# Optimization experiments

Measured on AMD Instinct MI355X. Metric: run time of the kernel, lower is better.

The kernel has to match this reference:

```python
import jax, jax.numpy as jnp
import numpy as np

N, E = 50000, 1600000
IN, OUT, H = 128, 32, 2
NT, ET = 20, 4
ETE, EAE, ED = 16, 16, 16
SLOPE = 0.2  # conv_neg_slope


def setup_inputs() -> dict:
    key = jax.random.key(0)
    ks = jax.random.split(key, 11)
    d_att = 2 * OUT + ETE + EAE
    return dict(
        x=jax.random.normal(ks[0], (N, IN), jnp.float32),
        edge_index=jax.random.randint(ks[1], (2, E), 0, N),
        ntypes=jax.random.randint(ks[2], (N,), 0, NT),
        etypes=jax.random.randint(ks[3], (E,), 0, ET),
        eattr=jax.random.normal(ks[4], (E, ED), jnp.float32),
        het_W=jax.random.normal(ks[5], (NT, IN, OUT), jnp.float32) / np.sqrt(IN).astype(np.float32),
        het_b=jnp.zeros((NT, OUT), jnp.float32),
        etype_table=jax.random.normal(ks[6], (ET, ETE), jnp.float32),
        eattr_W=jax.random.normal(ks[7], (ED, EAE), jnp.float32) / np.sqrt(ED).astype(np.float32),
        att_W=jax.random.normal(ks[8], (d_att, H), jnp.float32) / np.sqrt(d_att).astype(np.float32),
        lin_W=jax.random.normal(ks[9], (OUT + EAE, OUT), jnp.float32) / np.sqrt(OUT + EAE).astype(np.float32),
    )


def _lrelu(v):
    return jax.nn.leaky_relu(v, SLOPE)


def _heat_conv(x, edge_index, ntypes, etypes, eattr,
               het_W, het_b, etype_table, eattr_W, att_W, lin_W):
    # HeteroLinear: node-type-conditioned linear transform (loop over 20 types,
    # avoids materializing a [N, IN, OUT] gathered-weight tensor)
    h = jnp.zeros((x.shape[0], het_W.shape[-1]), x.dtype)
    for t in range(het_W.shape[0]):
        h = h + jnp.where((ntypes == t)[:, None], x @ het_W[t] + het_b[t], 0.0)

    src, dst = edge_index[0], edge_index[1]
    ete = _lrelu(etype_table[etypes])        # [E, ETE] edge-type embedding
    ea = _lrelu(eattr @ eattr_W)             # [E, EAE] edge-attr embedding
    x_i = h[dst]                             # target node feats [E, OUT]
    x_j = h[src]                             # source node feats [E, OUT]

    feat = jnp.concatenate([x_i, x_j, ete, ea], axis=-1)
    alpha = _lrelu(feat @ att_W)             # [E, H] raw attention logits

    # softmax grouped by destination node, per head
    amax = jax.ops.segment_max(alpha, dst, num_segments=N)  # [N, H]
    alpha = jnp.exp(alpha - amax[dst])
    denom = jax.ops.segment_sum(alpha, dst, num_segments=N)  # [N, H]
    alpha = alpha / denom[dst]

    msg = jnp.concatenate([x_j, ea], axis=-1) @ lin_W        # [E, OUT]
    m = (msg[:, None, :] * alpha[:, :, None]).reshape(alpha.shape[0], H * OUT)
    out = jax.ops.segment_sum(m, dst, num_segments=N)        # [N, H*OUT]
    return out  # concat=True -> flattened heads


def reference(x, edge_index, ntypes, etypes, eattr,
              het_W, het_b, etype_table, eattr_W, att_W, lin_W):
    out = _heat_conv(x, edge_index, ntypes, etypes, eattr,
                     het_W, het_b, etype_table, eattr_W, att_W, lin_W)
    return jax.nn.relu(out)  # final activation in forward (eval mode: no dropout)
```

## Files before the change

kernel.cpp:

```cpp
#include <hip/hip_runtime.h>
#include <hip/hip_fp16.h>

#define NN 50000
#define EE 1600000
#define IN_F 128
#define SLOPE 0.2f
#define NB_SCAN 196
#define NPAD 16

__global__ __launch_bounds__(256) void k_node(
    const float* __restrict__ x, const int* __restrict__ ntypes,
    const float* __restrict__ hetW, const float* __restrict__ hetb,
    const float* __restrict__ linW, const float* __restrict__ attW,
    float* __restrict__ hlin, float* __restrict__ auxS,
    float* __restrict__ auxD)
{
    __shared__ float sH[32 * 33];
    __shared__ float sLin[32 * 32];
    int tid = threadIdx.x;
    for (int i = tid; i < 1024; i += 256) sLin[i] = linW[i];

    int g = tid >> 3;
    int j = tid & 7;
    int n = blockIdx.x * 32 + g;
    int nc = n < NN ? n : NN - 1;
    int t = ntypes[nc];
    const float* W = hetW + (size_t)t * (IN_F * 32);
    const float4* xr = (const float4*)(x + (size_t)nc * IN_F);

    float4 acc = ((const float4*)(hetb + t * 32))[j];
    #pragma unroll 4
    for (int c = 0; c < 32; ++c) {
        float4 xv = xr[c];
        const float* Wr = W + (4 * c) * 32 + 4 * j;
        float4 w0 = *(const float4*)(Wr);
        float4 w1 = *(const float4*)(Wr + 32);
        float4 w2 = *(const float4*)(Wr + 64);
        float4 w3 = *(const float4*)(Wr + 96);
        acc.x += xv.x * w0.x + xv.y * w1.x + xv.z * w2.x + xv.w * w3.x;
        acc.y += xv.x * w0.y + xv.y * w1.y + xv.z * w2.y + xv.w * w3.y;
        acc.z += xv.x * w0.z + xv.y * w1.z + xv.z * w2.z + xv.w * w3.z;
        acc.w += xv.x * w0.w + xv.y * w1.w + xv.z * w2.w + xv.w * w3.w;
    }
    sH[g * 33 + 4 * j + 0] = acc.x;
    sH[g * 33 + 4 * j + 1] = acc.y;
    sH[g * 33 + 4 * j + 2] = acc.z;
    sH[g * 33 + 4 * j + 3] = acc.w;
    __syncthreads();

    int o = tid & 31;
    #pragma unroll
    for (int pass = 0; pass < 4; ++pass) {
        int g2 = (tid >> 5) + 8 * pass;
        int n2 = blockIdx.x * 32 + g2;
        if (n2 >= NN) break;
        float accl = 0.0f;
        #pragma unroll
        for (int k = 0; k < 32; ++k)
            accl += sH[g2 * 33 + k] * sLin[k * 32 + o];
        hlin[(size_t)n2 * 32 + o] = accl;

        float hv = sH[g2 * 33 + o];
        float p0 = hv * attW[o * 2],        p1 = hv * attW[o * 2 + 1];
        float p2 = hv * attW[(32 + o) * 2], p3 = hv * attW[(32 + o) * 2 + 1];
        #pragma unroll
        for (int m = 16; m >= 1; m >>= 1) {
            p0 += __shfl_xor(p0, m, 32);
            p1 += __shfl_xor(p1, m, 32);
            p2 += __shfl_xor(p2, m, 32);
            p3 += __shfl_xor(p3, m, 32);
        }
        if (o == 0) {
            auxD[n2 * 2] = p0; auxD[n2 * 2 + 1] = p1;
            auxS[n2 * 2] = p2; auxS[n2 * 2 + 1] = p3;
        }
    }
}

__global__ __launch_bounds__(256) void k_count(
    const int* __restrict__ dst, int* __restrict__ count)
{
    int e = blockIdx.x * 256 + threadIdx.x;
    atomicAdd(&count[dst[e]], 1);
}

__global__ __launch_bounds__(256) void k_scanA(
    const int* __restrict__ count, int* __restrict__ offsets,
    int* __restrict__ bsum)
{
    __shared__ int s[256];
    int t = threadIdx.x;
    int i = blockIdx.x * 256 + t;
    int c = (i < NN) ? count[i] : 0;
    s[t] = c;
    __syncthreads();
    for (int off = 1; off < 256; off <<= 1) {
        int v = (t >= off) ? s[t - off] : 0;
        __syncthreads();
        s[t] += v;
        __syncthreads();
    }
    if (i < NN) offsets[i] = s[t] - c;
    if (t == 255) bsum[blockIdx.x] = s[255];
}

__global__ __launch_bounds__(256) void k_scanB(
    const int* __restrict__ bsum, int* __restrict__ bbase,
    const float* __restrict__ etab, const float* __restrict__ attW,
    float* __restrict__ etedot)
{
    __shared__ int s[256];
    int t = threadIdx.x;
    if (t < 8) {
        int et = t >> 1, hh = t & 1;
        float acc = 0.0f;
        for (int k = 0; k < 16; ++k) {
            float v = etab[et * 16 + k];
            v = v > 0.0f ? v : SLOPE * v;
            acc += v * attW[(64 + k) * 2 + hh];
        }
        etedot[t] = acc;
    }
    int c = (t < NB_SCAN) ? bsum[t] : 0;
    s[t] = c;
    __syncthreads();
    for (int off = 1; off < 256; off <<= 1) {
        int v = (t >= off) ? s[t - off] : 0;
        __syncthreads();
        s[t] += v;
        __syncthreads();
    }
    if (t < NB_SCAN) bbase[t] = s[t] - c;
}

__global__ __launch_bounds__(256) void k_scanC(
    int* __restrict__ offsets, const int* __restrict__ bbase,
    int* __restrict__ nextPad)
{
    int t = threadIdx.x;
    int i = blockIdx.x * 256 + t;
    if (i < NN) {
        int v = offsets[i] + bbase[blockIdx.x];
        offsets[i] = v;
        nextPad[i * NPAD] = v;
    }
    if (i == 0) offsets[NN] = EE;
}

__global__ __launch_bounds__(256) void k_pre3(
    const int* __restrict__ srcp, const int* __restrict__ dstp,
    const int* __restrict__ etypes, const float* __restrict__ eattr,
    const float* __restrict__ eaW, const float* __restrict__ attW,
    const float* __restrict__ linW, const float* __restrict__ etedot,
    const float* __restrict__ auxS, const float* __restrict__ auxD,
    int* __restrict__ nextPad, __half* __restrict__ eaLinBuf,
    int2* __restrict__ recB)
{
    int e = blockIdx.x * 256 + threadIdx.x;
    int s = srcp[e], d = dstp[e], et = etypes[e];
    int slot = atomicAdd(&nextPad[d * NPAD], 1);

    float attr[16];
    {
        const float4* ap = (const float4*)(eattr + (size_t)e * 16);
        #pragma unroll
        for (int q = 0; q < 4; ++q) {
            float4 v = ap[q];
            attr[4*q+0] = v.x; attr[4*q+1] = v.y;
            attr[4*q+2] = v.z; attr[4*q+3] = v.w;
        }
    }
    float ea[16];
    #pragma unroll
    for (int j = 0; j < 16; ++j) {
        float acc = 0.0f;
        #pragma unroll
        for (int k = 0; k < 16; ++k) acc += attr[k] * eaW[k * 16 + j];
        ea[j] = acc > 0.0f ? acc : SLOPE * acc;
    }

    float2 aD = ((const float2*)auxD)[d];
    float2 aS = ((const float2*)auxS)[s];
    float2 eD = ((const float2*)etedot)[et];
    float al0 = aD.x + aS.x + eD.x;
    float al1 = aD.y + aS.y + eD.y;
    #pragma unroll
    for (int j = 0; j < 16; ++j) {
        al0 += ea[j] * attW[(80 + j) * 2];
        al1 += ea[j] * attW[(80 + j) * 2 + 1];
    }
    al0 = al0 > 0.0f ? al0 : SLOPE * al0;
    al1 = al1 > 0.0f ? al1 : SLOPE * al1;
    float p0 = __expf(al0), p1 = __expf(al1);

    float ml[32];
    #pragma unroll
    for (int o = 0; o < 32; ++o) ml[o] = 0.0f;
    #pragma unroll
    for (int j = 0; j < 16; ++j) {
        float ej = ea[j];
        #pragma unroll
        for (int o = 0; o < 32; ++o) ml[o] += ej * linW[(32 + j) * 32 + o];
    }

    __half2 mh[16];
    #pragma unroll
    for (int q = 0; q < 16; ++q)
        mh[q] = __floats2half2_rn(ml[2*q], ml[2*q+1]);
    float4* P = (float4*)(eaLinBuf + (size_t)slot * 32);
    const float4* ms = (const float4*)mh;
    #pragma unroll
    for (int q = 0; q < 4; ++q) P[q] = ms[q];

    __half2 ph = __floats2half2_rn(p0, p1);
    recB[slot] = make_int2(s, *(const int*)&ph);
}

__global__ __launch_bounds__(256) void k_gather3(
    const int* __restrict__ offsets, const __half* __restrict__ eaLinBuf,
    const int2* __restrict__ recB, const float* __restrict__ hlin,
    float* __restrict__ out)
{
    int tid = blockIdx.x * 256 + threadIdx.x;
    int n = tid >> 6;
    int lane = tid & 63;
    if (n >= NN) return;
    int o = lane & 31, hh = lane >> 5;
    int s0 = offsets[n], s1 = offsets[n + 1];

    float accm = 0.0f, accp = 0.0f;
    int slot = s0;
    for (; slot + 3 < s1; slot += 4) {
        int2 r0 = recB[slot + 0];
        int2 r1 = recB[slot + 1];
        int2 r2 = recB[slot + 2];
        int2 r3 = recB[slot + 3];
        float el0 = __half2float(eaLinBuf[(size_t)(slot + 0) * 32 + o]);
        float el1 = __half2float(eaLinBuf[(size_t)(slot + 1) * 32 + o]);
        float el2 = __half2float(eaLinBuf[(size_t)(slot + 2) * 32 + o]);
        float el3 = __half2float(eaLinBuf[(size_t)(slot + 3) * 32 + o]);
        float hv0 = hlin[(size_t)r0.x * 32 + o];
        float hv1 = hlin[(size_t)r1.x * 32 + o];
        float hv2 = hlin[(size_t)r2.x * 32 + o];
        float hv3 = hlin[(size_t)r3.x * 32 + o];
        __half2 q0 = *(const __half2*)&r0.y;
        __half2 q1 = *(const __half2*)&r1.y;
        __half2 q2 = *(const __half2*)&r2.y;
        __half2 q3 = *(const __half2*)&r3.y;
        float p0 = hh ? __high2float(q0) : __low2float(q0);
        float p1 = hh ? __high2float(q1) : __low2float(q1);
        float p2 = hh ? __high2float(q2) : __low2float(q2);
        float p3 = hh ? __high2float(q3) : __low2float(q3);
        accm += p0 * (hv0 + el0);
        accm += p1 * (hv1 + el1);
        accm += p2 * (hv2 + el2);
        accm += p3 * (hv3 + el3);
        accp += (p0 + p1) + (p2 + p3);
    }
    for (; slot < s1; ++slot) {
        int2 r = recB[slot];
        float el = __half2float(eaLinBuf[(size_t)slot * 32 + o]);
        float hv = hlin[(size_t)r.x * 32 + o];
        __half2 q = *(const __half2*)&r.y;
        float p = hh ? __high2float(q) : __low2float(q);
        accm += p * (hv + el);
        accp += p;
    }
    float v = accp > 0.0f ? accm / accp : 0.0f;
    out[(size_t)n * 64 + lane] = v > 0.0f ? v : 0.0f;
}

extern "C" void kernel_launch(void* const* d_in, const int* in_sizes, int n_in,
                              void* d_out, int out_size, void* d_ws, size_t ws_size,
                              hipStream_t stream)
{
    const float* x      = (const float*)d_in[0];
    const int*   eidx   = (const int*)  d_in[1];
    const int*   ntypes = (const int*)  d_in[2];
    const int*   etypes = (const int*)  d_in[3];
    const float* eattr  = (const float*)d_in[4];
    const float* hetW   = (const float*)d_in[5];
    const float* hetb   = (const float*)d_in[6];
    const float* etab   = (const float*)d_in[7];
    const float* eaW    = (const float*)d_in[8];
    const float* attW   = (const float*)d_in[9];
    const float* linW   = (const float*)d_in[10];
    float* out = (float*)d_out;

    char* ws = (char*)d_ws;
    size_t off = 0;
    auto alloc = [&](size_t bytes) {
        char* p = ws + off;
        off = (off + bytes + 255) & ~(size_t)255;
        return p;
    };
    float*  hlin     = (float*) alloc((size_t)NN * 32 * sizeof(float));
    float*  auxS     = (float*) alloc((size_t)NN * 2 * sizeof(float));
    float*  auxD     = (float*) alloc((size_t)NN * 2 * sizeof(float));
    float*  etedot   = (float*) alloc(8 * sizeof(float));
    int*    count    = (int*)   alloc((size_t)NN * sizeof(int));
    int*    offsets  = (int*)   alloc(((size_t)NN + 1) * sizeof(int));
    int*    nextPad  = (int*)   alloc((size_t)NN * NPAD * sizeof(int));
    int*    bsum     = (int*)   alloc(256 * sizeof(int));
    int*    bbase    = (int*)   alloc(256 * sizeof(int));
    int2*   recB     = (int2*)  alloc((size_t)EE * sizeof(int2));
    __half* eaLinBuf = (__half*)alloc((size_t)EE * 32 * sizeof(__half));
    (void)ws_size;

    const int* srcp = eidx;
    const int* dstp = eidx + EE;

    hipMemsetAsync(count, 0, (size_t)NN * sizeof(int), stream);

    k_node<<<(NN + 31) / 32, 256, 0, stream>>>(x, ntypes, hetW, hetb, linW,
                                               attW, hlin, auxS, auxD);
    k_count<<<EE / 256, 256, 0, stream>>>(dstp, count);
    k_scanA<<<NB_SCAN, 256, 0, stream>>>(count, offsets, bsum);
    k_scanB<<<1, 256, 0, stream>>>(bsum, bbase, etab, attW, etedot);
    k_scanC<<<NB_SCAN, 256, 0, stream>>>(offsets, bbase, nextPad);
    k_pre3<<<EE / 256, 256, 0, stream>>>(srcp, dstp, etypes, eattr, eaW, attW,
                                         linW, etedot, auxS, auxD, nextPad,
                                         eaLinBuf, recB);
    k_gather3<<<(NN * 64 + 255) / 256, 256, 0, stream>>>(offsets, eaLinBuf,
                                                         recB, hlin, out);
}
```

Baseline: 491.3 us.

## Store edge embedding instead of projected message; apply linW in gather via fdot2

The pre-pass now stores the 16-dim fp16 edge-attribute embedding plus the source index and attention weights in one 64-byte padded record per edge, instead of a 32-dim fp16 projected message and a separate 8-byte record. The gather kernel recomputes the eattr-to-message projection per lane with packed fp16 dot products, using linW columns held in registers. The aim is to shrink the scatter write and merge two streams into one aligned record, moving the projection arithmetic into the gather. The record is padded to 64 bytes, so the per-edge footprint stays close to before, and the fp16 weights add rounding error.

Result: slower. 577.8 us (+17.6%).

```diff
diff --git a/kernel.cpp b/kernel.cpp
--- a/kernel.cpp
+++ b/kernel.cpp
@@ -7,6 +7,8 @@
 #define SLOPE 0.2f
 #define NB_SCAN 196
 #define NPAD 16
+
+typedef _Float16 hf2 __attribute__((ext_vector_type(2)));
 
 __global__ __launch_bounds__(256) void k_node(
     const float* __restrict__ x, const int* __restrict__ ntypes,
@@ -147,14 +149,13 @@
     if (i == 0) offsets[NN] = EE;
 }
 
-__global__ __launch_bounds__(256) void k_pre3(
+__global__ __launch_bounds__(256) void k_pre4(
     const int* __restrict__ srcp, const int* __restrict__ dstp,
     const int* __restrict__ etypes, const float* __restrict__ eattr,
     const float* __restrict__ eaW, const float* __restrict__ attW,
-    const float* __restrict__ linW, const float* __restrict__ etedot,
-    const float* __restrict__ auxS, const float* __restrict__ auxD,
-    int* __restrict__ nextPad, __half* __restrict__ eaLinBuf,
-    int2* __restrict__ recB)
+    const float* __restrict__ etedot, const float* __restrict__ auxS,
+    const float* __restrict__ auxD, int* __restrict__ nextPad,
+    float4* __restrict__ recBuf)
 {
     int e = blockIdx.x * 256 + threadIdx.x;
     int s = srcp[e], d = dstp[e], et = etypes[e];
@@ -193,32 +194,27 @@
     al1 = al1 > 0.0f ? al1 : SLOPE * al1;
     float p0 = __expf(al0), p1 = __expf(al1);
 
-    float ml[32];
-    #pragma unroll
-    for (int o = 0; o < 32; ++o) ml[o] = 0.0f;
-    #pragma unroll
-    for (int j = 0; j < 16; ++j) {
-        float ej = ea[j];
-        #pragma unroll
-        for (int o = 0; o < 32; ++o) ml[o] += ej * linW[(32 + j) * 32 + o];
-    }
-
-    __half2 mh[16];
-    #pragma unroll
-    for (int q = 0; q < 16; ++q)
-        mh[q] = __floats2half2_rn(ml[2*q], ml[2*q+1]);
-    float4* P = (float4*)(eaLinBuf + (size_t)slot * 32);
-    const float4* ms = (const float4*)mh;
-    #pragma unroll
-    for (int q = 0; q < 4; ++q) P[q] = ms[q];
-
+    __half2 eh[8];
+    #pragma unroll
+    for (int q = 0; q < 8; ++q)
+        eh[q] = __floats2half2_rn(ea[2*q], ea[2*q+1]);
     __half2 ph = __floats2half2_rn(p0, p1);
-    recB[slot] = make_int2(s, *(const int*)&ph);
-}
-
-__global__ __launch_bounds__(256) void k_gather3(
-    const int* __restrict__ offsets, const __half* __restrict__ eaLinBuf,
-    const int2* __restrict__ recB, const float* __restrict__ hlin,
+
+    float4* P = recBuf + (size_t)slot * 4;
+    P[0] = ((const float4*)eh)[0];
+    P[1] = ((const float4*)eh)[1];
+    float4 m;
+    ((int*)&m)[0] = s;
+    ((int*)&m)[1] = *(const int*)&ph;
+    ((int*)&m)[2] = 0;
+    ((int*)&m)[3] = 0;
+    P[2] = m;
+    P[3] = make_float4(0.f, 0.f, 0.f, 0.f);
+}
+
+__global__ __launch_bounds__(256) void k_gather4(
+    const int* __restrict__ offsets, const float4* __restrict__ recBuf,
+    const float* __restrict__ hlin, const float* __restrict__ linW,
     float* __restrict__ out)
 {
     int tid = blockIdx.x * 256 + threadIdx.x;
@@ -226,45 +222,64 @@
     int lane = tid & 63;
     if (n >= NN) return;
     int o = lane & 31, hh = lane >> 5;
+
+    hf2 wcol[8];
+    #pragma unroll
+    for (int q = 0; q < 8; ++q) {
+        float wa = linW[(32 + 2 * q) * 32 + o];
+        float wb = linW[(33 + 2 * q) * 32 + o];
+        hf2 w; w[0] = (_Float16)wa; w[1] = (_Float16)wb;
+        wcol[q] = w;
+    }
+
     int s0 = offsets[n], s1 = offsets[n + 1];
-
     float accm = 0.0f, accp = 0.0f;
     int slot = s0;
-    for (; slot + 3 < s1; slot += 4) {
-        int2 r0 = recB[slot + 0];
-        int2 r1 = recB[slot + 1];
-        int2 r2 = recB[slot + 2];
-        int2 r3 = recB[slot + 3];
-        float el0 = __half2float(eaLinBuf[(size_t)(slot + 0) * 32 + o]);
-        float el1 = __half2float(eaLinBuf[(size_t)(slot + 1) * 32 + o]);
-        float el2 = __half2float(eaLinBuf[(size_t)(slot + 2) * 32 + o]);
-        float el3 = __half2float(eaLinBuf[(size_t)(slot + 3) * 32 + o]);
-        float hv0 = hlin[(size_t)r0.x * 32 + o];
-        float hv1 = hlin[(size_t)r1.x * 32 + o];
-        float hv2 = hlin[(size_t)r2.x * 32 + o];
-        float hv3 = hlin[(size_t)r3.x * 32 + o];
-        __half2 q0 = *(const __half2*)&r0.y;
-        __half2 q1 = *(const __half2*)&r1.y;
-        __half2 q2 = *(const __half2*)&r2.y;
-        __half2 q3 = *(const __half2*)&r3.y;
-        float p0 = hh ? __high2float(q0) : __low2float(q0);
-        float p1 = hh ? __high2float(q1) : __low2float(q1);
-        float p2 = hh ? __high2float(q2) : __low2float(q2);
-        float p3 = hh ? __high2float(q3) : __low2float(q3);
-        accm += p0 * (hv0 + el0);
-        accm += p1 * (hv1 + el1);
-        accm += p2 * (hv2 + el2);
-        accm += p3 * (hv3 + el3);
-        accp += (p0 + p1) + (p2 + p3);
+    for (; slot + 1 < s1; slot += 2) {
+        float4 a0 = recBuf[(size_t)slot * 4 + 0];
+        float4 a1 = recBuf[(size_t)slot * 4 + 1];
+        int2   ma = *(const int2*)(recBuf + (size_t)slot * 4 + 2);
+        float4 b0 = recBuf[(size_t)(slot + 1) * 4 + 0];
+        float4 b1 = recBuf[(size_t)(slot + 1) * 4 + 1];
+        int2   mb = *(const int2*)(recBuf + (size_t)(slot + 1) * 4 + 2);
+        float hva = hlin[(size_t)ma.x * 32 + o];
+        float hvb = hlin[(size_t)mb.x * 32 + o];
+
+        union { float4 f; hf2 h[4]; } ua0, ua1, ub0, ub1;
+        ua0.f = a0; ua1.f = a1; ub0.f = b0; ub1.f = b1;
+        float ea0 = 0.f, ea1 = 0.f, eb0 = 0.f, eb1 = 0.f;
+        #pragma unroll
+        for (int q = 0; q < 4; ++q) {
+            ea0 = __builtin_amdgcn_fdot2(ua0.h[q], wcol[q],     ea0, false);
+            ea1 = __builtin_amdgcn_fdot2(ua1.h[q], wcol[4 + q], ea1, false);
+            eb0 = __builtin_amdgcn_fdot2(ub0.h[q], wcol[q],     eb0, false);
+            eb1 = __builtin_amdgcn_fdot2(ub1.h[q], wcol[4 + q], eb1, false);
+        }
+        __half2 qa = *(const __half2*)&ma.y;
+        __half2 qb = *(const __half2*)&mb.y;
+        float pa = hh ? __high2float(qa) : __low2float(qa);
+        float pb = hh ? __high2float(qb) : __low2float(qb);
+        accm += pa * (hva + ea0 + ea1);
+        accm += pb * (hvb + eb0 + eb1);
+        accp += pa + pb;
     }
     for (; slot < s1; ++slot) {
-        int2 r = recB[slot];
-        float el = __half2float(eaLinBuf[(size_t)slot * 32 + o]);
-        float hv = hlin[(size_t)r.x * 32 + o];
-        __half2 q = *(const __half2*)&r.y;
-        float p = hh ? __high2float(q) : __low2float(q);
-        accm += p * (hv + el);
-        accp += p;
+        float4 a0 = recBuf[(size_t)slot * 4 + 0];
+        float4 a1 = recBuf[(size_t)slot * 4 + 1];
+        int2   ma = *(const int2*)(recBuf + (size_t)slot * 4 + 2);
+        float hva = hlin[(size_t)ma.x * 32 + o];
+        union { float4 f; hf2 h[4]; } ua0, ua1;
+        ua0.f = a0; ua1.f = a1;
+        float e0 = 0.f, e1 = 0.f;
+        #pragma unroll
+        for (int q = 0; q < 4; ++q) {
+            e0 = __builtin_amdgcn_fdot2(ua0.h[q], wcol[q],     e0, false);
+            e1 = __builtin_amdgcn_fdot2(ua1.h[q], wcol[4 + q], e1, false);
+        }
+        __half2 qa = *(const __half2*)&ma.y;
+        float pa = hh ? __high2float(qa) : __low2float(qa);
+        accm += pa * (hva + e0 + e1);
+        accp += pa;
     }
     float v = accp > 0.0f ? accm / accp : 0.0f;
     out[(size_t)n * 64 + lane] = v > 0.0f ? v : 0.0f;
@@ -303,8 +318,7 @@
     int*    nextPad  = (int*)   alloc((size_t)NN * NPAD * sizeof(int));
     int*    bsum     = (int*)   alloc(256 * sizeof(int));
     int*    bbase    = (int*)   alloc(256 * sizeof(int));
-    int2*   recB     = (int2*)  alloc((size_t)EE * sizeof(int2));
-    __half* eaLinBuf = (__half*)alloc((size_t)EE * 32 * sizeof(__half));
+    float4* recBuf   = (float4*)alloc((size_t)EE * 64);
     (void)ws_size;
 
     const int* srcp = eidx;
@@ -318,9 +332,8 @@
     k_scanA<<<NB_SCAN, 256, 0, stream>>>(count, offsets, bsum);
     k_scanB<<<1, 256, 0, stream>>>(bsum, bbase, etab, attW, etedot);
     k_scanC<<<NB_SCAN, 256, 0, stream>>>(offsets, bbase, nextPad);
-    k_pre3<<<EE / 256, 256, 0, stream>>>(srcp, dstp, etypes, eattr, eaW, attW,
-                                         linW, etedot, auxS, auxD, nextPad,
-                                         eaLinBuf, recB);
-    k_gather3<<<(NN * 64 + 255) / 256, 256, 0, stream>>>(offsets, eaLinBuf,
-                                                         recB, hlin, out);
-}
+    k_pre4<<<EE / 256, 256, 0, stream>>>(srcp, dstp, etypes, eattr, eaW, attW,
+                                         etedot, auxS, auxD, nextPad, recBuf);
+    k_gather4<<<(NN * 64 + 255) / 256, 256, 0, stream>>>(offsets, recBuf,
+                                                         hlin, linW, out);
+}
```
